# Kernel optimization log

Hardware: AMD Instinct MI355X
Metric: run time of the kernel (lower is better)

## Reference

```python
import jax, jax.numpy as jnp
import numpy as np

N0, N1, N2 = 120000, 30000, 6000   # node frontier sizes per hop
E0, E1 = 480000, 96000             # sampled edges per layer (~fanout 16)
D = 128                            # in_channels == hidden_size
R = 8                              # num_relations
NB = 4                             # num_bases
ETOT = 3000000                     # global edge count (edge_type_all)


def setup_inputs() -> dict:
    key = jax.random.key(0)
    ks = jax.random.split(key, 24)
    s = 1.0 / np.sqrt(D)
    f32 = jnp.float32
    inp = {
        "x": jax.random.normal(ks[0], (N0, D), dtype=f32),
        "src0": jax.random.randint(ks[1], (E0,), 0, N0),
        "dst0": jax.random.randint(ks[2], (E0,), 0, N1),
        "e_id0": jax.random.randint(ks[3], (E0,), 0, ETOT),
        "src1": jax.random.randint(ks[4], (E1,), 0, N1),
        "dst1": jax.random.randint(ks[5], (E1,), 0, N2),
        "e_id1": jax.random.randint(ks[6], (E1,), 0, ETOT),
        "edge_type_all": jax.random.randint(ks[7], (ETOT,), 0, R),
        # pre_layer: linear + relu
        "pre_W": jax.random.normal(ks[8], (D, D), dtype=f32) * s,
        "pre_b": jnp.zeros((D,), f32),
        # RGCNConv layer 0 (basis decomposition)
        "basis0": jax.random.normal(ks[9], (NB, D, D), dtype=f32) * s,
        "comp0": jax.random.normal(ks[10], (R, NB), dtype=f32) * (1.0 / np.sqrt(NB)),
        "root0": jax.random.normal(ks[11], (D, D), dtype=f32) * s,
        "bias0": jnp.zeros((D,), f32),
        "g0": jnp.ones((D,), f32),
        "be0": jnp.zeros((D,), f32),
        # RGCNConv layer 1
        "basis1": jax.random.normal(ks[12], (NB, D, D), dtype=f32) * s,
        "comp1": jax.random.normal(ks[13], (R, NB), dtype=f32) * (1.0 / np.sqrt(NB)),
        "root1": jax.random.normal(ks[14], (D, D), dtype=f32) * s,
        "bias1": jnp.zeros((D,), f32),
        "g1": jnp.ones((D,), f32),
        "be1": jnp.zeros((D,), f32),
        # post_layer: single linear
        "post_W": jax.random.normal(ks[15], (D, D), dtype=f32) * s,
        "post_b": jnp.zeros((D,), f32),
    }
    return inp


def _layernorm(x, g, b, eps=1e-5):
    mu = jnp.mean(x, axis=-1, keepdims=True)
    var = jnp.mean(jnp.square(x - mu), axis=-1, keepdims=True)
    return (x - mu) * jax.lax.rsqrt(var + eps) * g + b


def _rgcn_conv(x, n_dst, src, dst, etype, basis, comp, root, bias):
    # Bipartite RGCNConv with basis decomposition and mean aggregation.
    # Since messages W[r] @ x[src] are linear, aggregate per relation first
    # (segment_sum of raw features), then apply the relation weight once.
    x_t = x[:n_dst]                                    # [n_dst, D]
    out = x_t @ root + bias                            # root/self transform
    W = jnp.einsum('rb,bio->rio', comp, basis)         # [R, D, D]
    x_j = x[src]                                       # [E, D] gather
    deg = jax.ops.segment_sum(jnp.ones(src.shape[0], x.dtype), dst,
                              num_segments=n_dst)      # mean over all relations
    agg = jnp.zeros((n_dst, W.shape[-1]), x.dtype)
    for r in range(W.shape[0]):                        # R=8 structurally distinct
        m = (etype == r).astype(x.dtype)[:, None]
        s_r = jax.ops.segment_sum(x_j * m, dst, num_segments=n_dst)
        agg = agg + s_r @ W[r]
    return out + agg / jnp.maximum(deg, 1.0)[:, None]


def reference(x, src0, dst0, e_id0, src1, dst1, e_id1, edge_type_all,
              pre_W, pre_b, basis0, comp0, root0, bias0, g0, be0,
              basis1, comp1, root1, bias1, g1, be1, post_W, post_b):
    # pre_layer: linear + relu (GeneralMultiLayer, final_act=True)
    h = jax.nn.relu(x @ pre_W + pre_b)
    # layer 0: edge-type gather -> relational conv -> norm -> act (eval: no dropout)
    h = _rgcn_conv(h, N1, src0, dst0, edge_type_all[e_id0],
                   basis0, comp0, root0, bias0)
    h = jax.nn.relu(_layernorm(h, g0, be0))
    # layer 1
    h = _rgcn_conv(h, N2, src1, dst1, edge_type_all[e_id1],
                   basis1, comp1, root1, bias1)
    h = jax.nn.relu(_layernorm(h, g1, be1))
    # post_layer: single linear MLP
    return h @ post_W + post_b
```

## Files before the change

### kernel.cpp

```cpp
#include <hip/hip_runtime.h>
#include <cstdint>

#define DD 128
#define CAP 64
#define E0C 480000
#define E1C 96000
#define N0C 120000
#define N1C 30000
#define N2C 6000
#define ETOTC 3000000

typedef unsigned short u16;
typedef __attribute__((ext_vector_type(8))) short bf16x8;
typedef __attribute__((ext_vector_type(16))) float f32x16;

__device__ __forceinline__ u16 f2b(float f) {
    union { float f; unsigned u; } a; a.f = f;
    unsigned r = (a.u + 0x7fffu + ((a.u >> 16) & 1u)) >> 16;
    return (u16)r;
}
__device__ __forceinline__ float b2f(u16 u) {
    union { unsigned u; float f; } a; a.u = ((unsigned)u) << 16;
    return a.f;
}

struct WtJob { const float* src[12]; };
__global__ __launch_bounds__(256) void prep_kernel(
    WtJob job, u16* __restrict__ dst, int* __restrict__ cnt0, int* __restrict__ cnt1,
    const int* __restrict__ etype, unsigned* __restrict__ r4)
{
    int gtid = blockIdx.x * 256 + threadIdx.x;
    for (int i = gtid; i < N1C + N2C; i += 256 * 256) {
        if (i < N1C) cnt0[i] = 0; else cnt1[i - N1C] = 0;
    }
    for (int i = gtid; i < ETOTC / 8; i += 256 * 256) {
        int4 a = ((const int4*)etype)[i * 2];
        int4 b = ((const int4*)etype)[i * 2 + 1];
        unsigned p = (unsigned)(a.x & 7) | ((unsigned)(a.y & 7) << 4)
                   | ((unsigned)(a.z & 7) << 8) | ((unsigned)(a.w & 7) << 12)
                   | ((unsigned)(b.x & 7) << 16) | ((unsigned)(b.y & 7) << 20)
                   | ((unsigned)(b.z & 7) << 24) | ((unsigned)(b.w & 7) << 28);
        r4[i] = p;
    }
    if (blockIdx.x >= 192) return;
    __shared__ float tile[32][33];
    int m = blockIdx.x >> 4;
    int t4 = blockIdx.x & 15;
    int tr = (t4 >> 2) * 32;
    int tc = (t4 & 3) * 32;
    int lx = threadIdx.x & 31, ly = threadIdx.x >> 5;
    #pragma unroll
    for (int yy = 0; yy < 32; yy += 8)
        tile[ly + yy][lx] = job.src[m][(tr + ly + yy) * DD + tc + lx];
    __syncthreads();
    int tid = threadIdx.x;
    if (tid < 128) {
        int nl = tid >> 2, kch = tid & 3;
        int k = tr + kch * 8, n = tc + nl;
        int kc = k >> 4, half = (k >> 3) & 1;
        int t = n >> 5, l31 = n & 31;
        bf16x8 pk;
        #pragma unroll
        for (int j = 0; j < 8; ++j) pk[j] = (short)f2b(tile[kch * 8 + j][nl]);
        *(bf16x8*)(dst + (size_t)m * 16384 + kc * 2048 + t * 512 + half * 256 + l31 * 8) = pk;
    }
}

__global__ __launch_bounds__(256) void fill_kernel(
    const int* __restrict__ src0, const int* __restrict__ dst0, const int* __restrict__ eid0,
    const int* __restrict__ src1, const int* __restrict__ dst1, const int* __restrict__ eid1,
    const unsigned* __restrict__ r4,
    int* __restrict__ cnt0, int* __restrict__ cnt1,
    int* __restrict__ ep0, int* __restrict__ ep1)
{
    int idx = blockIdx.x * 256 + threadIdx.x;
    bool L0 = idx < E0C;
    int ee = L0 ? idx : idx - E0C;
    if (ee >= (L0 ? E0C : E1C)) return;
    int s   = L0 ? src0[ee] : src1[ee];
    int d   = L0 ? dst0[ee] : dst1[ee];
    int eid = L0 ? eid0[ee] : eid1[ee];
    int r = (int)((r4[eid >> 3] >> ((eid & 7) << 2)) & 7u);
    int pos = atomicAdd((L0 ? cnt0 : cnt1) + d, 1);
    if (pos < CAP)
        (L0 ? ep0 : ep1)[(size_t)d * CAP + pos] = s | (r << 28);
}

__global__ __launch_bounds__(256) void pre_gemm_kernel(
    const float* __restrict__ x, const u16* __restrict__ Wr,
    const float* __restrict__ bias, u16* __restrict__ h0)
{
    int wave = threadIdx.x >> 6;
    int lane = threadIdx.x & 63;
    int l31 = lane & 31, half = lane >> 5;
    int m0 = (blockIdx.x * 4 + wave) * 32;
    if (m0 >= N0C) return;
    int arow = m0 + l31;
    bool rv = arow < N0C;

    const float* Aq = x + (size_t)arow * DD;
    float4 st[16];
    if (rv) {
        #pragma unroll
        for (int c = 0; c < 16; ++c)
            st[c] = *(const float4*)(Aq + ((c >> 1) * 16 + half * 8) + (c & 1) * 4);
    } else {
        #pragma unroll
        for (int c = 0; c < 16; ++c) st[c] = make_float4(0.f, 0.f, 0.f, 0.f);
    }
    f32x16 accs[4];
    #pragma unroll
    for (int t = 0; t < 4; ++t)
        #pragma unroll
        for (int i = 0; i < 16; ++i) accs[t][i] = 0.f;
    #pragma unroll
    for (int kc = 0; kc < 8; ++kc) {
        bf16x8 bfr[4];
        #pragma unroll
        for (int t = 0; t < 4; ++t)
            bfr[t] = *(const bf16x8*)(Wr + (size_t)((kc * 4 + t) * 64 + lane) * 8);
        float4 u0 = st[2 * kc], u1 = st[2 * kc + 1];
        bf16x8 af;
        af[0] = (short)f2b(u0.x); af[1] = (short)f2b(u0.y);
        af[2] = (short)f2b(u0.z); af[3] = (short)f2b(u0.w);
        af[4] = (short)f2b(u1.x); af[5] = (short)f2b(u1.y);
        af[6] = (short)f2b(u1.z); af[7] = (short)f2b(u1.w);
        #pragma unroll
        for (int t = 0; t < 4; ++t)
            accs[t] = __builtin_amdgcn_mfma_f32_32x32x16_bf16(af, bfr[t], accs[t], 0, 0, 0);
    }
    float bb[4];
    #pragma unroll
    for (int t = 0; t < 4; ++t) bb[t] = bias[t * 32 + l31];
    #pragma unroll
    for (int reg = 0; reg < 16; ++reg) {
        int rl = (reg & 3) + 8 * (reg >> 2) + 4 * half;
        int row = m0 + rl;
        if (row < N0C) {
            #pragma unroll
            for (int t = 0; t < 4; ++t)
                h0[(size_t)row * DD + t * 32 + l31] =
                    f2b(fmaxf(accs[t][reg] + bb[t], 0.f));
        }
    }
}

__global__ __launch_bounds__(256) void agg_kernel(
    const u16* __restrict__ h, const int* __restrict__ cnt,
    const int* __restrict__ ep, const float* __restrict__ comp,
    u16* __restrict__ T, int ndst)
{
    __shared__ float4 cmp4[8];
    if (threadIdx.x < 8) cmp4[threadIdx.x] = ((const float4*)comp)[threadIdx.x];
    __syncthreads();
    int row = blockIdx.x * 4 + (threadIdx.x >> 6);
    if (row >= ndst) return;
    int lane = threadIdx.x & 63;
    int n = cnt[row];
    int end = n < CAP ? n : CAP;
    const int* erow = ep + (size_t)row * CAP;
    float a0[4] = {0.f, 0.f, 0.f, 0.f};
    float a1[4] = {0.f, 0.f, 0.f, 0.f};
    int j = 0;
    for (; j + 16 <= end; j += 16) {
        int vv[16]; unsigned gg[16];
        #pragma unroll
        for (int u = 0; u < 16; ++u) vv[u] = erow[j + u];
        #pragma unroll
        for (int u = 0; u < 16; ++u)
            gg[u] = *(const unsigned*)(h + (size_t)(vv[u] & 0x0FFFFFFF) * DD + 2 * lane);
        #pragma unroll
        for (int u = 0; u < 16; ++u) {
            float4 c = cmp4[vv[u] >> 28];
            float x0 = b2f((u16)(gg[u] & 0xffffu));
            float x1 = b2f((u16)(gg[u] >> 16));
            a0[0] = fmaf(c.x, x0, a0[0]); a1[0] = fmaf(c.x, x1, a1[0]);
            a0[1] = fmaf(c.y, x0, a0[1]); a1[1] = fmaf(c.y, x1, a1[1]);
            a0[2] = fmaf(c.z, x0, a0[2]); a1[2] = fmaf(c.z, x1, a1[2]);
            a0[3] = fmaf(c.w, x0, a0[3]); a1[3] = fmaf(c.w, x1, a1[3]);
        }
    }
    for (; j + 4 <= end; j += 4) {
        int vv[4]; unsigned gg[4];
        #pragma unroll
        for (int u = 0; u < 4; ++u) vv[u] = erow[j + u];
        #pragma unroll
        for (int u = 0; u < 4; ++u)
            gg[u] = *(const unsigned*)(h + (size_t)(vv[u] & 0x0FFFFFFF) * DD + 2 * lane);
        #pragma unroll
        for (int u = 0; u < 4; ++u) {
            float4 c = cmp4[vv[u] >> 28];
            float x0 = b2f((u16)(gg[u] & 0xffffu));
            float x1 = b2f((u16)(gg[u] >> 16));
            a0[0] = fmaf(c.x, x0, a0[0]); a1[0] = fmaf(c.x, x1, a1[0]);
            a0[1] = fmaf(c.y, x0, a0[1]); a1[1] = fmaf(c.y, x1, a1[1]);
            a0[2] = fmaf(c.z, x0, a0[2]); a1[2] = fmaf(c.z, x1, a1[2]);
            a0[3] = fmaf(c.w, x0, a0[3]); a1[3] = fmaf(c.w, x1, a1[3]);
        }
    }
    for (; j < end; ++j) {
        int v = erow[j];
        unsigned g = *(const unsigned*)(h + (size_t)(v & 0x0FFFFFFF) * DD + 2 * lane);
        float4 c = cmp4[v >> 28];
        float x0 = b2f((u16)(g & 0xffffu));
        float x1 = b2f((u16)(g >> 16));
        a0[0] = fmaf(c.x, x0, a0[0]); a1[0] = fmaf(c.x, x1, a1[0]);
        a0[1] = fmaf(c.y, x0, a0[1]); a1[1] = fmaf(c.y, x1, a1[1]);
        a0[2] = fmaf(c.z, x0, a0[2]); a1[2] = fmaf(c.z, x1, a1[2]);
        a0[3] = fmaf(c.w, x0, a0[3]); a1[3] = fmaf(c.w, x1, a1[3]);
    }
    float inv = 1.f / fmaxf((float)n, 1.f);
    #pragma unroll
    for (int b = 0; b < 4; ++b) {
        unsigned pk = (unsigned)f2b(a0[b] * inv) | ((unsigned)f2b(a1[b] * inv) << 16);
        *(unsigned*)(T + ((size_t)b * ndst + row) * DD + 2 * lane) = pk;
    }
}

template<bool OBF16, bool LN>
__global__ __launch_bounds__(64) void mfma_gemm(
    const u16* __restrict__ Ap, int nplanes, const u16* __restrict__ Ar,
    const u16* __restrict__ Wp, const u16* __restrict__ Wr,
    const float* __restrict__ bias, const float* __restrict__ gw,
    const float* __restrict__ bw, void* __restrict__ Cv, int nrows)
{
    int lane = threadIdx.x & 63;
    int l31 = lane & 31, half = lane >> 5;
    int m0 = blockIdx.x * 32;
    int arow = m0 + l31;
    bool rv = arow < nrows;
    f32x16 acc[4];
    #pragma unroll
    for (int t = 0; t < 4; ++t)
        #pragma unroll
        for (int i = 0; i < 16; ++i) acc[t][i] = 0.f;

    bf16x8 A0[8], A1[8];
    {
        const u16* Ainit = (nplanes == 0) ? Ar : Ap;
        if (rv) {
            #pragma unroll
            for (int c = 0; c < 8; ++c)
                A0[c] = *(const bf16x8*)(Ainit + (size_t)arow * DD + c * 16 + half * 8);
        } else {
            #pragma unroll
            for (int c = 0; c < 8; ++c) A0[c] = (bf16x8){0,0,0,0,0,0,0,0};
        }
    }
    for (int p = 0; p <= nplanes; ++p) {
        const u16* Wsel = (p == nplanes) ? Wr : Wp + p * 16384;
        if (p < nplanes) {
            const u16* An = (p + 1 == nplanes) ? Ar : Ap + (size_t)(p + 1) * nrows * DD;
            if (rv) {
                #pragma unroll
                for (int c = 0; c < 8; ++c)
                    A1[c] = *(const bf16x8*)(An + (size_t)arow * DD + c * 16 + half * 8);
            } else {
                #pragma unroll
                for (int c = 0; c < 8; ++c) A1[c] = (bf16x8){0,0,0,0,0,0,0,0};
            }
        }
        #pragma unroll
        for (int kc = 0; kc < 8; ++kc) {
            bf16x8 bfr[4];
            #pragma unroll
            for (int t = 0; t < 4; ++t)
                bfr[t] = *(const bf16x8*)(Wsel + (size_t)((kc * 4 + t) * 64 + lane) * 8);
            #pragma unroll
            for (int t = 0; t < 4; ++t)
                acc[t] = __builtin_amdgcn_mfma_f32_32x32x16_bf16(A0[kc], bfr[t], acc[t], 0, 0, 0);
        }
        if (p < nplanes) {
            #pragma unroll
            for (int c = 0; c < 8; ++c) A0[c] = A1[c];
        }
    }

    float bb[4];
    #pragma unroll
    for (int t = 0; t < 4; ++t) bb[t] = bias[t * 32 + l31];
    float gg[4], ww[4];
    if (LN) {
        #pragma unroll
        for (int t = 0; t < 4; ++t) { gg[t] = gw[t * 32 + l31]; ww[t] = bw[t * 32 + l31]; }
    }

    #pragma unroll
    for (int reg = 0; reg < 16; ++reg) {
        int rl = (reg & 3) + 8 * (reg >> 2) + 4 * half;
        int row = m0 + rl;
        float v[4];
        #pragma unroll
        for (int t = 0; t < 4; ++t) v[t] = acc[t][reg] + bb[t];
        if (LN) {
            float s1 = 0.f, s2 = 0.f;
            #pragma unroll
            for (int t = 0; t < 4; ++t) { s1 += v[t]; s2 += v[t] * v[t]; }
            #pragma unroll
            for (int o = 1; o < 32; o <<= 1) {
                s1 += __shfl_xor(s1, o);
                s2 += __shfl_xor(s2, o);
            }
            float mu = s1 * (1.f / 128.f);
            float var = s2 * (1.f / 128.f) - mu * mu;
            float rstd = rsqrtf(fmaxf(var, 0.f) + 1e-5f);
            #pragma unroll
            for (int t = 0; t < 4; ++t)
                v[t] = fmaxf((v[t] - mu) * rstd * gg[t] + ww[t], 0.f);
        }
        if (row < nrows) {
            #pragma unroll
            for (int t = 0; t < 4; ++t) {
                if (OBF16) ((u16*)Cv)[(size_t)row * DD + t * 32 + l31] = f2b(v[t]);
                else       ((float*)Cv)[(size_t)row * DD + t * 32 + l31] = v[t];
            }
        }
    }
}

extern "C" void kernel_launch(void* const* d_in, const int* in_sizes, int n_in,
                              void* d_out, int out_size, void* d_ws, size_t ws_size,
                              hipStream_t stream)
{
    const float* x     = (const float*)d_in[0];
    const int* src0    = (const int*)d_in[1];
    const int* dst0    = (const int*)d_in[2];
    const int* eid0    = (const int*)d_in[3];
    const int* src1    = (const int*)d_in[4];
    const int* dst1    = (const int*)d_in[5];
    const int* eid1    = (const int*)d_in[6];
    const int* etype   = (const int*)d_in[7];
    const float* preW  = (const float*)d_in[8];
    const float* preb  = (const float*)d_in[9];
    const float* basis0 = (const float*)d_in[10];
    const float* comp0  = (const float*)d_in[11];
    const float* root0  = (const float*)d_in[12];
    const float* bias0  = (const float*)d_in[13];
    const float* g0    = (const float*)d_in[14];
    const float* be0   = (const float*)d_in[15];
    const float* basis1 = (const float*)d_in[16];
    const float* comp1  = (const float*)d_in[17];
    const float* root1  = (const float*)d_in[18];
    const float* bias1  = (const float*)d_in[19];
    const float* g1    = (const float*)d_in[20];
    const float* be1   = (const float*)d_in[21];
    const float* postW = (const float*)d_in[22];
    const float* postb = (const float*)d_in[23];
    float* out = (float*)d_out;

    char* ws = (char*)d_ws;
    size_t o = 0;
    auto alloc = [&](size_t bytes) { char* p = ws + o; o += (bytes + 255) & ~(size_t)255; return p; };
    u16* h0   = (u16*)alloc((size_t)N0C * DD * 2);
    u16* T0   = (u16*)alloc((size_t)4 * N1C * DD * 2);
    u16* h1   = (u16*)alloc((size_t)N1C * DD * 2);
    u16* T1   = (u16*)alloc((size_t)4 * N2C * DD * 2);
    u16* h2   = (u16*)alloc((size_t)N2C * DD * 2);
    u16* wt   = (u16*)alloc((size_t)12 * 16384 * 2);
    int* cnt0 = (int*)alloc((size_t)N1C * 4);
    int* cnt1 = (int*)alloc((size_t)N2C * 4);
    int* ep0  = (int*)alloc((size_t)N1C * CAP * 4);
    int* ep1  = (int*)alloc((size_t)N2C * CAP * 4);
    unsigned* r4 = (unsigned*)alloc((size_t)(ETOTC / 8) * 4);

    WtJob job;
    job.src[0] = preW;
    for (int b = 0; b < 4; ++b) job.src[1 + b] = basis0 + (size_t)b * 16384;
    job.src[5] = root0;
    for (int b = 0; b < 4; ++b) job.src[6 + b] = basis1 + (size_t)b * 16384;
    job.src[10] = root1;
    job.src[11] = postW;

    prep_kernel<<<256, 256, 0, stream>>>(job, wt, cnt0, cnt1, etype, r4);
    fill_kernel<<<(E0C + E1C) / 256, 256, 0, stream>>>(
        src0, dst0, eid0, src1, dst1, eid1, r4, cnt0, cnt1, ep0, ep1);
    pre_gemm_kernel<<<(N0C + 127) / 128, 256, 0, stream>>>(
        x, wt + 0 * 16384, preb, h0);
    agg_kernel<<<(N1C + 3) / 4, 256, 0, stream>>>(h0, cnt0, ep0, comp0, T0, N1C);
    mfma_gemm<true, true><<<(N1C + 31) / 32, 64, 0, stream>>>(
        T0, 4, h0, wt + 1 * 16384, wt + 5 * 16384, bias0, g0, be0, h1, N1C);
    agg_kernel<<<(N2C + 3) / 4, 256, 0, stream>>>(h1, cnt1, ep1, comp1, T1, N2C);
    mfma_gemm<true, true><<<(N2C + 31) / 32, 64, 0, stream>>>(
        T1, 4, h1, wt + 6 * 16384, wt + 10 * 16384, bias1, g1, be1, h2, N2C);
    mfma_gemm<false, false><<<(N2C + 31) / 32, 64, 0, stream>>>(
        nullptr, 0, h2, nullptr, wt + 11 * 16384, postb, nullptr, nullptr, out, N2C);
}
```

Before: 303.4 us.

## Fuse aggregation with basis GEMM and partition edge fill by destination range

The edge aggregation is fused with the basis/root MFMA GEMM and LayerNorm into a single kernel. Each wave aggregates 8 destination rows into shared memory and then runs MFMA on a 32-row tile with only 8 valid rows, which removes the T0/T1 intermediate round trip through global memory. The fill kernel now has each block read a slice of edges and handle only one of 8 destination partitions, aiming to localise atomics and scatter writes. The cost is that every edge is read 8 times, and the GEMM wastes 3/4 of its MFMA work while each wave reloads all weights.

```diff
diff --git a/kernel.cpp b/kernel.cpp
--- a/kernel.cpp
+++ b/kernel.cpp
@@ -9,6 +9,7 @@
 #define N1C 30000
 #define N2C 6000
 #define ETOTC 3000000
+#define FSLICE 2250
 
 typedef unsigned short u16;
 typedef __attribute__((ext_vector_type(8))) short bf16x8;
@@ -73,17 +74,25 @@
     int* __restrict__ cnt0, int* __restrict__ cnt1,
     int* __restrict__ ep0, int* __restrict__ ep1)
 {
-    int idx = blockIdx.x * 256 + threadIdx.x;
-    bool L0 = idx < E0C;
-    int ee = L0 ? idx : idx - E0C;
-    if (ee >= (L0 ? E0C : E1C)) return;
-    int s   = L0 ? src0[ee] : src1[ee];
-    int d   = L0 ? dst0[ee] : dst1[ee];
-    int eid = L0 ? eid0[ee] : eid1[ee];
-    int r = (int)((r4[eid >> 3] >> ((eid & 7) << 2)) & 7u);
-    int pos = atomicAdd((L0 ? cnt0 : cnt1) + d, 1);
-    if (pos < CAP)
-        (L0 ? ep0 : ep1)[(size_t)d * CAP + pos] = s | (r << 28);
+    int part  = blockIdx.x & 7;
+    int slice = blockIdx.x >> 3;
+    int lo0 = part * (N1C / 8), hi0 = lo0 + N1C / 8;
+    int lo1 = part * (N2C / 8), hi1 = lo1 + N2C / 8;
+    int base = slice * FSLICE;
+    for (int t = threadIdx.x; t < FSLICE; t += 256) {
+        int idx = base + t;
+        bool L0 = idx < E0C;
+        int ee = L0 ? idx : idx - E0C;
+        int d   = L0 ? dst0[ee] : dst1[ee];
+        int s   = L0 ? src0[ee] : src1[ee];
+        int eid = L0 ? eid0[ee] : eid1[ee];
+        bool mine = L0 ? (d >= lo0 && d < hi0) : (d >= lo1 && d < hi1);
+        if (!mine) continue;
+        int r = (int)((r4[eid >> 3] >> ((eid & 7) << 2)) & 7u);
+        int pos = atomicAdd((L0 ? cnt0 : cnt1) + d, 1);
+        if (pos < CAP)
+            (L0 ? ep0 : ep1)[(size_t)d * CAP + pos] = s | (r << 28);
+    }
 }
 
 __global__ __launch_bounds__(256) void pre_gemm_kernel(
@@ -145,75 +154,171 @@
     }
 }
 
-__global__ __launch_bounds__(256) void agg_kernel(
+__global__ __launch_bounds__(256) void aggemm_kernel(
     const u16* __restrict__ h, const int* __restrict__ cnt,
     const int* __restrict__ ep, const float* __restrict__ comp,
-    u16* __restrict__ T, int ndst)
-{
-    __shared__ float4 cmp4[8];
-    if (threadIdx.x < 8) cmp4[threadIdx.x] = ((const float4*)comp)[threadIdx.x];
+    const u16* __restrict__ Wp, const u16* __restrict__ Wr,
+    const float* __restrict__ bias, const float* __restrict__ gw,
+    const float* __restrict__ bw, u16* __restrict__ Cout, int ndst)
+{
+    __shared__ u16 lt[4][4][8][136];
+    __shared__ float4 cmp4s[8];
+    if (threadIdx.x < 8) cmp4s[threadIdx.x] = ((const float4*)comp)[threadIdx.x];
     __syncthreads();
-    int row = blockIdx.x * 4 + (threadIdx.x >> 6);
-    if (row >= ndst) return;
-    int lane = threadIdx.x & 63;
-    int n = cnt[row];
-    int end = n < CAP ? n : CAP;
-    const int* erow = ep + (size_t)row * CAP;
-    float a0[4] = {0.f, 0.f, 0.f, 0.f};
-    float a1[4] = {0.f, 0.f, 0.f, 0.f};
-    int j = 0;
-    for (; j + 16 <= end; j += 16) {
-        int vv[16]; unsigned gg[16];
-        #pragma unroll
-        for (int u = 0; u < 16; ++u) vv[u] = erow[j + u];
-        #pragma unroll
-        for (int u = 0; u < 16; ++u)
-            gg[u] = *(const unsigned*)(h + (size_t)(vv[u] & 0x0FFFFFFF) * DD + 2 * lane);
-        #pragma unroll
-        for (int u = 0; u < 16; ++u) {
-            float4 c = cmp4[vv[u] >> 28];
-            float x0 = b2f((u16)(gg[u] & 0xffffu));
-            float x1 = b2f((u16)(gg[u] >> 16));
-            a0[0] = fmaf(c.x, x0, a0[0]); a1[0] = fmaf(c.x, x1, a1[0]);
-            a0[1] = fmaf(c.y, x0, a0[1]); a1[1] = fmaf(c.y, x1, a1[1]);
-            a0[2] = fmaf(c.z, x0, a0[2]); a1[2] = fmaf(c.z, x1, a1[2]);
-            a0[3] = fmaf(c.w, x0, a0[3]); a1[3] = fmaf(c.w, x1, a1[3]);
-        }
-    }
-    for (; j + 4 <= end; j += 4) {
-        int vv[4]; unsigned gg[4];
-        #pragma unroll
-        for (int u = 0; u < 4; ++u) vv[u] = erow[j + u];
-        #pragma unroll
-        for (int u = 0; u < 4; ++u)
-            gg[u] = *(const unsigned*)(h + (size_t)(vv[u] & 0x0FFFFFFF) * DD + 2 * lane);
-        #pragma unroll
-        for (int u = 0; u < 4; ++u) {
-            float4 c = cmp4[vv[u] >> 28];
-            float x0 = b2f((u16)(gg[u] & 0xffffu));
-            float x1 = b2f((u16)(gg[u] >> 16));
-            a0[0] = fmaf(c.x, x0, a0[0]); a1[0] = fmaf(c.x, x1, a1[0]);
-            a0[1] = fmaf(c.y, x0, a0[1]); a1[1] = fmaf(c.y, x1, a1[1]);
-            a0[2] = fmaf(c.z, x0, a0[2]); a1[2] = fmaf(c.z, x1, a1[2]);
-            a0[3] = fmaf(c.w, x0, a0[3]); a1[3] = fmaf(c.w, x1, a1[3]);
-        }
-    }
-    for (; j < end; ++j) {
-        int v = erow[j];
-        unsigned g = *(const unsigned*)(h + (size_t)(v & 0x0FFFFFFF) * DD + 2 * lane);
-        float4 c = cmp4[v >> 28];
-        float x0 = b2f((u16)(g & 0xffffu));
-        float x1 = b2f((u16)(g >> 16));
-        a0[0] = fmaf(c.x, x0, a0[0]); a1[0] = fmaf(c.x, x1, a1[0]);
-        a0[1] = fmaf(c.y, x0, a0[1]); a1[1] = fmaf(c.y, x1, a1[1]);
-        a0[2] = fmaf(c.z, x0, a0[2]); a1[2] = fmaf(c.z, x1, a1[2]);
-        a0[3] = fmaf(c.w, x0, a0[3]); a1[3] = fmaf(c.w, x1, a1[3]);
-    }
-    float inv = 1.f / fmaxf((float)n, 1.f);
-    #pragma unroll
-    for (int b = 0; b < 4; ++b) {
-        unsigned pk = (unsigned)f2b(a0[b] * inv) | ((unsigned)f2b(a1[b] * inv) << 16);
-        *(unsigned*)(T + ((size_t)b * ndst + row) * DD + 2 * lane) = pk;
+
+    int wave = threadIdx.x >> 6, lane = threadIdx.x & 63;
+    int l31 = lane & 31, half = lane >> 5;
+    int rbase = (blockIdx.x * 4 + wave) * 8;
+    if (rbase >= ndst) return;
+
+    for (int rr = 0; rr < 8; ++rr) {
+        int row = rbase + rr;
+        float a0[4] = {0.f, 0.f, 0.f, 0.f};
+        float a1[4] = {0.f, 0.f, 0.f, 0.f};
+        int n = 0;
+        if (row < ndst) {
+            n = cnt[row];
+            int end = n < CAP ? n : CAP;
+            const int* erow = ep + (size_t)row * CAP;
+            int j = 0;
+            for (; j + 16 <= end; j += 16) {
+                int vv[16]; unsigned gg[16];
+                #pragma unroll
+                for (int u = 0; u < 16; ++u) vv[u] = erow[j + u];
+                #pragma unroll
+                for (int u = 0; u < 16; ++u)
+                    gg[u] = *(const unsigned*)(h + (size_t)(vv[u] & 0x0FFFFFFF) * DD + 2 * lane);
+                #pragma unroll
+                for (int u = 0; u < 16; ++u) {
+                    float4 c = cmp4s[vv[u] >> 28];
+                    float x0 = b2f((u16)(gg[u] & 0xffffu));
+                    float x1 = b2f((u16)(gg[u] >> 16));
+                    a0[0] = fmaf(c.x, x0, a0[0]); a1[0] = fmaf(c.x, x1, a1[0]);
+                    a0[1] = fmaf(c.y, x0, a0[1]); a1[1] = fmaf(c.y, x1, a1[1]);
+                    a0[2] = fmaf(c.z, x0, a0[2]); a1[2] = fmaf(c.z, x1, a1[2]);
+                    a0[3] = fmaf(c.w, x0, a0[3]); a1[3] = fmaf(c.w, x1, a1[3]);
+                }
+            }
+            for (; j + 4 <= end; j += 4) {
+                int vv[4]; unsigned gg[4];
+                #pragma unroll
+                for (int u = 0; u < 4; ++u) vv[u] = erow[j + u];
+                #pragma unroll
+                for (int u = 0; u < 4; ++u)
+                    gg[u] = *(const unsigned*)(h + (size_t)(vv[u] & 0x0FFFFFFF) * DD + 2 * lane);
+                #pragma unroll
+                for (int u = 0; u < 4; ++u) {
+                    float4 c = cmp4s[vv[u] >> 28];
+                    float x0 = b2f((u16)(gg[u] & 0xffffu));
+                    float x1 = b2f((u16)(gg[u] >> 16));
+                    a0[0] = fmaf(c.x, x0, a0[0]); a1[0] = fmaf(c.x, x1, a1[0]);
+                    a0[1] = fmaf(c.y, x0, a0[1]); a1[1] = fmaf(c.y, x1, a1[1]);
+                    a0[2] = fmaf(c.z, x0, a0[2]); a1[2] = fmaf(c.z, x1, a1[2]);
+                    a0[3] = fmaf(c.w, x0, a0[3]); a1[3] = fmaf(c.w, x1, a1[3]);
+                }
+            }
+            for (; j < end; ++j) {
+                int v = erow[j];
+                unsigned g = *(const unsigned*)(h + (size_t)(v & 0x0FFFFFFF) * DD + 2 * lane);
+                float4 c = cmp4s[v >> 28];
+                float x0 = b2f((u16)(g & 0xffffu));
+                float x1 = b2f((u16)(g >> 16));
+                a0[0] = fmaf(c.x, x0, a0[0]); a1[0] = fmaf(c.x, x1, a1[0]);
+                a0[1] = fmaf(c.y, x0, a0[1]); a1[1] = fmaf(c.y, x1, a1[1]);
+                a0[2] = fmaf(c.z, x0, a0[2]); a1[2] = fmaf(c.z, x1, a1[2]);
+                a0[3] = fmaf(c.w, x0, a0[3]); a1[3] = fmaf(c.w, x1, a1[3]);
+            }
+        }
+        float inv = 1.f / fmaxf((float)n, 1.f);
+        #pragma unroll
+        for (int b = 0; b < 4; ++b) {
+            unsigned pk = (unsigned)f2b(a0[b] * inv) | ((unsigned)f2b(a1[b] * inv) << 16);
+            *(unsigned*)&lt[wave][b][rr][2 * lane] = pk;
+        }
+    }
+
+    f32x16 acc[4];
+    #pragma unroll
+    for (int t = 0; t < 4; ++t)
+        #pragma unroll
+        for (int i = 0; i < 16; ++i) acc[t][i] = 0.f;
+
+    #pragma unroll
+    for (int p = 0; p < 4; ++p) {
+        bf16x8 A[8];
+        #pragma unroll
+        for (int c = 0; c < 8; ++c) {
+            if (l31 < 8)
+                A[c] = *(const bf16x8*)&lt[wave][p][l31][c * 16 + half * 8];
+            else
+                A[c] = (bf16x8){0,0,0,0,0,0,0,0};
+        }
+        const u16* W = Wp + (size_t)p * 16384;
+        #pragma unroll
+        for (int kc = 0; kc < 8; ++kc) {
+            bf16x8 bfr[4];
+            #pragma unroll
+            for (int t = 0; t < 4; ++t)
+                bfr[t] = *(const bf16x8*)(W + (size_t)((kc * 4 + t) * 64 + lane) * 8);
+            #pragma unroll
+            for (int t = 0; t < 4; ++t)
+                acc[t] = __builtin_amdgcn_mfma_f32_32x32x16_bf16(A[kc], bfr[t], acc[t], 0, 0, 0);
+        }
+    }
+    {
+        bf16x8 A[8];
+        int arow = rbase + l31;
+        if (l31 < 8 && arow < ndst) {
+            #pragma unroll
+            for (int c = 0; c < 8; ++c)
+                A[c] = *(const bf16x8*)(h + (size_t)arow * DD + c * 16 + half * 8);
+        } else {
+            #pragma unroll
+            for (int c = 0; c < 8; ++c) A[c] = (bf16x8){0,0,0,0,0,0,0,0};
+        }
+        #pragma unroll
+        for (int kc = 0; kc < 8; ++kc) {
+            bf16x8 bfr[4];
+            #pragma unroll
+            for (int t = 0; t < 4; ++t)
+                bfr[t] = *(const bf16x8*)(Wr + (size_t)((kc * 4 + t) * 64 + lane) * 8);
+            #pragma unroll
+            for (int t = 0; t < 4; ++t)
+                acc[t] = __builtin_amdgcn_mfma_f32_32x32x16_bf16(A[kc], bfr[t], acc[t], 0, 0, 0);
+        }
+    }
+
+    float bb[4], gg4[4], ww4[4];
+    #pragma unroll
+    for (int t = 0; t < 4; ++t) {
+        bb[t] = bias[t * 32 + l31];
+        gg4[t] = gw[t * 32 + l31];
+        ww4[t] = bw[t * 32 + l31];
+    }
+    #pragma unroll
+    for (int reg = 0; reg < 4; ++reg) {
+        int rl = reg + 4 * half;
+        int row = rbase + rl;
+        float v[4];
+        #pragma unroll
+        for (int t = 0; t < 4; ++t) v[t] = acc[t][reg] + bb[t];
+        float s1 = 0.f, s2 = 0.f;
+        #pragma unroll
+        for (int t = 0; t < 4; ++t) { s1 += v[t]; s2 += v[t] * v[t]; }
+        #pragma unroll
+        for (int o = 1; o < 32; o <<= 1) {
+            s1 += __shfl_xor(s1, o);
+            s2 += __shfl_xor(s2, o);
+        }
+        float mu = s1 * (1.f / 128.f);
+        float var = s2 * (1.f / 128.f) - mu * mu;
+        float rstd = rsqrtf(fmaxf(var, 0.f) + 1e-5f);
+        if (row < ndst) {
+            #pragma unroll
+            for (int t = 0; t < 4; ++t)
+                Cout[(size_t)row * DD + t * 32 + l31] =
+                    f2b(fmaxf((v[t] - mu) * rstd * gg4[t] + ww4[t], 0.f));
+        }
     }
 }
 
@@ -352,9 +457,7 @@
     size_t o = 0;
     auto alloc = [&](size_t bytes) { char* p = ws + o; o += (bytes + 255) & ~(size_t)255; return p; };
     u16* h0   = (u16*)alloc((size_t)N0C * DD * 2);
-    u16* T0   = (u16*)alloc((size_t)4 * N1C * DD * 2);
     u16* h1   = (u16*)alloc((size_t)N1C * DD * 2);
-    u16* T1   = (u16*)alloc((size_t)4 * N2C * DD * 2);
     u16* h2   = (u16*)alloc((size_t)N2C * DD * 2);
     u16* wt   = (u16*)alloc((size_t)12 * 16384 * 2);
     int* cnt0 = (int*)alloc((size_t)N1C * 4);
@@ -372,16 +475,16 @@
     job.src[11] = postW;
 
     prep_kernel<<<256, 256, 0, stream>>>(job, wt, cnt0, cnt1, etype, r4);
-    fill_kernel<<<(E0C + E1C) / 256, 256, 0, stream>>>(
+    fill_kernel<<<2048, 256, 0, stream>>>(
         src0, dst0, eid0, src1, dst1, eid1, r4, cnt0, cnt1, ep0, ep1);
     pre_gemm_kernel<<<(N0C + 127) / 128, 256, 0, stream>>>(
         x, wt + 0 * 16384, preb, h0);
-    agg_kernel<<<(N1C + 3) / 4, 256, 0, stream>>>(h0, cnt0, ep0, comp0, T0, N1C);
-    mfma_gemm<true, true><<<(N1C + 31) / 32, 64, 0, stream>>>(
-        T0, 4, h0, wt + 1 * 16384, wt + 5 * 16384, bias0, g0, be0, h1, N1C);
-    agg_kernel<<<(N2C + 3) / 4, 256, 0, stream>>>(h1, cnt1, ep1, comp1, T1, N2C);
-    mfma_gemm<true, true><<<(N2C + 31) / 32, 64, 0, stream>>>(
-        T1, 4, h1, wt + 6 * 16384, wt + 10 * 16384, bias1, g1, be1, h2, N2C);
+    aggemm_kernel<<<(N1C + 31) / 32, 256, 0, stream>>>(
+        h0, cnt0, ep0, comp0, wt + 1 * 16384, wt + 5 * 16384,
+        bias0, g0, be0, h1, N1C);
+    aggemm_kernel<<<(N2C + 31) / 32, 256, 0, stream>>>(
+        h1, cnt1, ep1, comp1, wt + 6 * 16384, wt + 10 * 16384,
+        bias1, g1, be1, h2, N2C);
     mfma_gemm<false, false><<<(N2C + 31) / 32, 64, 0, stream>>>(
         nullptr, 0, h2, nullptr, wt + 11 * 16384, postb, nullptr, nullptr, out, N2C);
 }
```

Result: slower. 320.5 us (+5.6%).
